# Performance work log

Hardware: AMD Instinct MI355X
Metric: run time of the kernel (lower is better)

## Reference

```python
import jax, jax.numpy as jnp
import numpy as np

WS = 4      # window_size (RSUT5 default)
SHIFT = 2   # window_size // 2
NH = 8      # num_heads
DIM = 256
H0 = W0 = T0 = 32
B0 = 1


def _ln(x, g, b, eps=1e-5):
    m = x.mean(-1, keepdims=True)
    v = ((x - m) ** 2).mean(-1, keepdims=True)
    return (x - m) / jnp.sqrt(v + eps) * g + b


def _rel_index(ws):
    c = np.stack(np.meshgrid(np.arange(ws), np.arange(ws), np.arange(ws), indexing='ij')).reshape(3, -1)
    r = (c[:, :, None] - c[:, None, :]).transpose(1, 2, 0) + (ws - 1)
    return jnp.asarray((r[..., 0] * (2 * ws - 1) + r[..., 1]) * (2 * ws - 1) + r[..., 2])


def _partition(x, ws):
    B, H, W, T, C = x.shape
    x = x.reshape(B, H // ws, ws, W // ws, ws, T // ws, ws, C)
    return x.transpose(0, 1, 3, 5, 2, 4, 6, 7).reshape(-1, ws ** 3, C)


def _reverse(w, ws, B, H, W, T):
    C = w.shape[-1]
    x = w.reshape(B, H // ws, W // ws, T // ws, ws, ws, ws, C)
    return x.transpose(0, 1, 4, 2, 5, 3, 6, 7).reshape(B, H, W, T, C)


def _attn_mask(H, W, T, ws, ss):
    # static (numpy) replica of Block.createmask; H,W,T divisible by ws here
    img = np.zeros((H, W, T), np.float32)
    sls = (slice(0, -ws), slice(-ws, -ss), slice(-ss, None))
    cnt = 0
    for h in sls:
        for w in sls:
            for t in sls:
                img[h, w, t] = cnt
                cnt += 1
    mw = img.reshape(H // ws, ws, W // ws, ws, T // ws, ws).transpose(0, 2, 4, 1, 3, 5).reshape(-1, ws ** 3)
    d = mw[:, None, :] - mw[:, :, None]
    return jnp.asarray(np.where(d != 0, -100.0, 0.0).astype(np.float32))


def _swin(x, H, W, T, shift, mask, n1g, n1b, qkvw, qkvb, rpb, projw, projb, n2g, n2b, fc1w, fc1b, fc2w, fc2b):
    B, L, C = x.shape
    N = WS ** 3
    hd = C // NH
    shortcut = x
    x = _ln(x, n1g, n1b).reshape(B, H, W, T, C)
    if shift:
        x = jnp.roll(x, (-shift, -shift, -shift), axis=(1, 2, 3))
    xw = _partition(x, WS)                                        # [B*nW, N, C]
    qkv = (xw @ qkvw.T + qkvb).reshape(-1, N, 3, NH, hd).transpose(2, 0, 3, 1, 4)
    q, k, v = qkv[0], qkv[1], qkv[2]                              # [B*nW, NH, N, hd]
    attn = jnp.einsum('bhnd,bhmd->bhnm', q * (hd ** -0.5), k)
    attn = attn + rpb[_rel_index(WS)].transpose(2, 0, 1)[None]    # relative position bias
    if mask is not None:
        nW = mask.shape[0]
        attn = (attn.reshape(B, nW, NH, N, N) + mask[None, :, None]).reshape(-1, NH, N, N)
    attn = jax.nn.softmax(attn, axis=-1)
    out = jnp.einsum('bhnm,bhmd->bhnd', attn, v).transpose(0, 2, 1, 3).reshape(-1, N, C)
    out = out @ projw.T + projb
    x = _reverse(out, WS, B, H, W, T)
    if shift:
        x = jnp.roll(x, (shift, shift, shift), axis=(1, 2, 3))
    x = shortcut + x.reshape(B, L, C)
    h = _ln(x, n2g, n2b)
    h = jax.nn.gelu(h @ fc1w.T + fc1b, approximate=False) @ fc2w.T + fc2b
    return x + h


def setup_inputs() -> dict:
    key = jax.random.key(0)
    ks = iter(jax.random.split(key, 16))
    def rn(shape, s=0.02):
        return jax.random.normal(next(ks), shape, jnp.float32) * s
    d = {'x': jax.random.normal(next(ks), (B0, H0 * W0 * T0, DIM), jnp.float32),
         'H': H0, 'W': W0, 'T': T0,
         'norm_g': jnp.ones((DIM,), jnp.float32), 'norm_b': jnp.zeros((DIM,), jnp.float32)}
    for p in ('w', 's'):
        d[p + 'n1g'] = jnp.ones((DIM,), jnp.float32); d[p + 'n1b'] = jnp.zeros((DIM,), jnp.float32)
        d[p + 'qkvw'] = rn((3 * DIM, DIM)); d[p + 'qkvb'] = jnp.zeros((3 * DIM,), jnp.float32)
        d[p + 'rpb'] = rn(((2 * WS - 1) ** 3, NH))
        d[p + 'projw'] = rn((DIM, DIM)); d[p + 'projb'] = jnp.zeros((DIM,), jnp.float32)
        d[p + 'n2g'] = jnp.ones((DIM,), jnp.float32); d[p + 'n2b'] = jnp.zeros((DIM,), jnp.float32)
        d[p + 'fc1w'] = rn((4 * DIM, DIM)); d[p + 'fc1b'] = jnp.zeros((4 * DIM,), jnp.float32)
        d[p + 'fc2w'] = rn((DIM, 4 * DIM)); d[p + 'fc2b'] = jnp.zeros((DIM,), jnp.float32)
    return d


def reference(x, H, W, T, norm_g, norm_b,
              wn1g, wn1b, wqkvw, wqkvb, wrpb, wprojw, wprojb, wn2g, wn2b, wfc1w, wfc1b, wfc2w, wfc2b,
              sn1g, sn1b, sqkvw, sqkvb, srpb, sprojw, sprojb, sn2g, sn2b, sfc1w, sfc1b, sfc2w, sfc2b):
    mask = _attn_mask(H, W, T, WS, SHIFT)
    x = _swin(x, H, W, T, 0, None, wn1g, wn1b, wqkvw, wqkvb, wrpb, wprojw, wprojb, wn2g, wn2b, wfc1w, wfc1b, wfc2w, wfc2b)
    x = _swin(x, H, W, T, SHIFT, mask, sn1g, sn1b, sqkvw, sqkvb, srpb, sprojw, sprojb, sn2g, sn2b, sfc1w, sfc1b, sfc2w, sfc2b)
    B, L, C = x.shape
    # Block.norm + toConv: [B, L, C] -> [B, C, H, W, T]
    return _ln(x, norm_g, norm_b).reshape(B, H, W, T, C).transpose(0, 4, 1, 2, 3)
```

## Files before the change

kernel.cpp:

```cpp
#include <hip/hip_runtime.h>

typedef unsigned short u16;
typedef unsigned int   u32;
typedef __bf16 bfx8 __attribute__((ext_vector_type(8)));
typedef float  fx4  __attribute__((ext_vector_type(4)));

__device__ __forceinline__ u16 f2b(float f) {
    union { float f; u32 i; } v; v.f = f;
    u32 r = (v.i + 0x7fffu + ((v.i >> 16) & 1u)) >> 16;
    return (u16)r;
}
__device__ __forceinline__ u32 pk(float a, float b) {
    return (u32)f2b(a) | ((u32)f2b(b) << 16);
}

__device__ __forceinline__ void gl2lds16(const u16* g, u16* l) {
    __builtin_amdgcn_global_load_lds(
        (const __attribute__((address_space(1))) u32*)(const void*)g,
        (__attribute__((address_space(3))) u32*)(void*)l, 16, 0, 0);
}

__device__ __forceinline__ int map_token(int r, int shift) {
    int win = r >> 6, n = r & 63;
    int wh = win >> 6, ww = (win >> 3) & 7, wt = win & 7;
    int h = wh * 4 + (n >> 4);
    int w = ww * 4 + ((n >> 2) & 3);
    int t = wt * 4 + (n & 3);
    h = (h + shift) & 31; w = (w + shift) & 31; t = (t + shift) & 31;
    return (h << 10) | (w << 5) | t;
}

struct CvtArgs { const float* src[8]; int cum[9]; };
__global__ __launch_bounds__(256) void cvt_kernel(CvtArgs a, u16* __restrict__ dst) {
    int g = (blockIdx.x * 256 + threadIdx.x) * 4;
    int t = 0;
    #pragma unroll
    for (int i = 1; i < 8; i++) t += (g >= a.cum[i]);
    int local = g - a.cum[t];
    float4 f = *(const float4*)(a.src[t] + local);
    uint2 o; o.x = pk(f.x, f.y); o.y = pk(f.z, f.w);
    *(uint2*)(dst + g) = o;
}

template<int GATHER, int F32OUT>
__global__ __launch_bounds__(256) void ln_kernel(const float* __restrict__ resid,
                                                 const float* __restrict__ g, const float* __restrict__ b,
                                                 void* __restrict__ outp, int shift) {
    int lane = threadIdx.x & 63;
    int row  = blockIdx.x * 4 + (threadIdx.x >> 6);
    int src  = GATHER ? map_token(row, shift) : row;
    float4 x = ((const float4*)(resid + src * 256))[lane];
    float s1 = x.x + x.y + x.z + x.w;
    float s2 = x.x * x.x + x.y * x.y + x.z * x.z + x.w * x.w;
    #pragma unroll
    for (int off = 1; off < 64; off <<= 1) { s1 += __shfl_xor(s1, off); s2 += __shfl_xor(s2, off); }
    float mean = s1 * (1.0f / 256.0f);
    float var  = s2 * (1.0f / 256.0f) - mean * mean;
    float rstd = rsqrtf(var + 1e-5f);
    int c = lane * 4;
    float4 gv = *(const float4*)(g + c);
    float4 bv = *(const float4*)(b + c);
    float y0 = (x.x - mean) * rstd * gv.x + bv.x;
    float y1 = (x.y - mean) * rstd * gv.y + bv.y;
    float y2 = (x.z - mean) * rstd * gv.z + bv.z;
    float y3 = (x.w - mean) * rstd * gv.w + bv.w;
    if (F32OUT) {
        float4 o; o.x = y0; o.y = y1; o.z = y2; o.w = y3;
        *(float4*)((float*)outp + row * 256 + c) = o;
    } else {
        uint2 o; o.x = pk(y0, y1); o.y = pk(y2, y3);
        *(uint2*)((u16*)outp + row * 256 + c) = o;
    }
}

template<int EPI>
__global__ __launch_bounds__(256) void gemm2(const u16* __restrict__ A, const u16* __restrict__ W,
                                             const float* __restrict__ bias,
                                             u16* __restrict__ outb, float* __restrict__ resid,
                                             int Nout, int K, int shift) {
    __shared__ u16 As[128 * 32];
    __shared__ u16 Bs[128 * 32];
    int lane = threadIdx.x & 63, w = threadIdx.x >> 6;
    int wm = w >> 1, wn = w & 1;
    int m0 = blockIdx.x * 128, n0 = blockIdx.y * 128;
    int lr = lane & 15, q = lane >> 4;
    int sw = q ^ ((lr >> 1) & 3);

    fx4 acc[4][4] = {};

    for (int kt = 0; kt < K; kt += 32) {
        __syncthreads();
        #pragma unroll
        for (int p = 0; p < 2; p++) {
            int row = p * 64 + w * 16 + (lane >> 2);
            int kg  = (lane & 3) ^ ((row >> 1) & 3);
            int slot = (p * 256 + w * 64 + lane) * 8;
            gl2lds16(A + (size_t)(m0 + row) * K + kt + kg * 8, As + slot);
            gl2lds16(W + (size_t)(n0 + row) * K + kt + kg * 8, Bs + slot);
        }
        __syncthreads();
        bfx8 af[4], bfr[4];
        #pragma unroll
        for (int t = 0; t < 4; t++) {
            int ra = wm * 64 + t * 16 + lr;
            int rb = wn * 64 + t * 16 + lr;
            af[t]  = *(const bfx8*)(As + (ra * 4 + sw) * 8);
            bfr[t] = *(const bfx8*)(Bs + (rb * 4 + sw) * 8);
        }
        #pragma unroll
        for (int i = 0; i < 4; i++)
            #pragma unroll
            for (int j = 0; j < 4; j++)
                acc[i][j] = __builtin_amdgcn_mfma_f32_16x16x32_bf16(af[i], bfr[j], acc[i][j], 0, 0, 0);
    }

    float bv[4];
    #pragma unroll
    for (int j = 0; j < 4; j++) bv[j] = bias[n0 + wn * 64 + j * 16 + lr];
    #pragma unroll
    for (int i = 0; i < 4; i++) {
        #pragma unroll
        for (int r = 0; r < 4; r++) {
            int gr = m0 + wm * 64 + i * 16 + q * 4 + r;
            int orow = (EPI == 3) ? map_token(gr, shift) : gr;
            #pragma unroll
            for (int j = 0; j < 4; j++) {
                int gc = n0 + wn * 64 + j * 16 + lr;
                float v = acc[i][j][r] + bv[j];
                if (EPI == 0) {
                    outb[(size_t)gr * Nout + gc] = f2b(v);
                } else if (EPI == 1) {
                    float gl = 0.5f * v * (1.0f + erff(v * 0.7071067811865476f));
                    outb[(size_t)gr * Nout + gc] = f2b(gl);
                } else {
                    resid[orow * 256 + gc] += v;
                }
            }
        }
    }
}

__global__ __launch_bounds__(128) void attn_mfma(const u16* __restrict__ qkv, const float* __restrict__ rpb,
                                                 u16* __restrict__ outb, int masked) {
    __shared__ u16  Pl[2][64][72];
    __shared__ u16  VT[2][32][72];
    __shared__ float rbS[2][344];
    int w = threadIdx.x >> 6;
    int lane = threadIdx.x & 63;
    int id = blockIdx.x * 2 + w;
    int win = id >> 3, head = id & 7;
    int lr = lane & 15, q = lane >> 4;

    const u16* base = qkv + (size_t)win * 64 * 768 + head * 32;

    bfx8 qf[4], kf[4];
    #pragma unroll
    for (int t = 0; t < 4; t++) {
        const u16* rq = base + (lr + 16 * t) * 768 + q * 8;
        qf[t] = *(const bfx8*)(rq);
        kf[t] = *(const bfx8*)(rq + 256);
    }
    {
        const u16* rv = base + lane * 768 + 512;
        #pragma unroll
        for (int c = 0; c < 32; c += 8) {
            bfx8 vv = *(const bfx8*)(rv + c);
            #pragma unroll
            for (int j = 0; j < 8; j++) VT[w][c + j][lane] = ((const u16*)&vv)[j];
        }
    }
    for (int i = lane; i < 343; i += 64) rbS[w][i] = rpb[i * 8 + head];

    fx4 sT[4][4] = {};
    #pragma unroll
    for (int jt = 0; jt < 4; jt++)
        #pragma unroll
        for (int it = 0; it < 4; it++)
            sT[jt][it] = __builtin_amdgcn_mfma_f32_16x16x32_bf16(kf[jt], qf[it], sT[jt][it], 0, 0, 0);

    int wh = win >> 6, ww = (win >> 3) & 7, wt = win & 7;
    const float scale = 0.17677669529663687f;

    #pragma unroll
    for (int it = 0; it < 4; it++) {
        int i = lr + 16 * it;
        int ih = i >> 4, iw = (i >> 2) & 3, iT = i & 3;
        int labn = 0;
        if (masked) {
            int lh = (wh == 7) ? (1 + (ih >> 1)) : 0;
            int lw = (ww == 7) ? (1 + (iw >> 1)) : 0;
            int lt = (wt == 7) ? (1 + (iT >> 1)) : 0;
            labn = lh * 9 + lw * 3 + lt;
        }
        float sv[4][4];
        float mx = -1e30f;
        #pragma unroll
        for (int jt = 0; jt < 4; jt++)
            #pragma unroll
            for (int r = 0; r < 4; r++) {
                int j = q * 4 + r + 16 * jt;
                int jh = j >> 4, jw = (j >> 2) & 3, jT = j & 3;
                float s = sT[jt][it][r] * scale +
                          rbS[w][((ih - jh + 3) * 7 + (iw - jw + 3)) * 7 + (iT - jT + 3)];
                if (masked) {
                    int lh = (wh == 7) ? (1 + (jh >> 1)) : 0;
                    int lw = (ww == 7) ? (1 + (jw >> 1)) : 0;
                    int lt = (wt == 7) ? (1 + (jT >> 1)) : 0;
                    if (lh * 9 + lw * 3 + lt != labn) s -= 100.0f;
                }
                sv[jt][r] = s;
                mx = fmaxf(mx, s);
            }
        mx = fmaxf(mx, __shfl_xor(mx, 16));
        mx = fmaxf(mx, __shfl_xor(mx, 32));
        float sum = 0.f;
        #pragma unroll
        for (int jt = 0; jt < 4; jt++)
            #pragma unroll
            for (int r = 0; r < 4; r++) { sv[jt][r] = __expf(sv[jt][r] - mx); sum += sv[jt][r]; }
        sum += __shfl_xor(sum, 16);
        sum += __shfl_xor(sum, 32);
        float inv = 1.0f / sum;
        #pragma unroll
        for (int jt = 0; jt < 4; jt++) {
            uint2 pw;
            pw.x = pk(sv[jt][0] * inv, sv[jt][1] * inv);
            pw.y = pk(sv[jt][2] * inv, sv[jt][3] * inv);
            *(uint2*)&Pl[w][i][q * 4 + 16 * jt] = pw;
        }
    }

    fx4 o[4][2] = {};
    #pragma unroll
    for (int kk = 0; kk < 2; kk++) {
        bfx8 pf[4], vf[2];
        #pragma unroll
        for (int it = 0; it < 4; it++) pf[it] = *(const bfx8*)&Pl[w][lr + 16 * it][q * 8 + 32 * kk];
        #pragma unroll
        for (int dt = 0; dt < 2; dt++) vf[dt] = *(const bfx8*)&VT[w][lr + 16 * dt][q * 8 + 32 * kk];
        #pragma unroll
        for (int it = 0; it < 4; it++)
            #pragma unroll
            for (int dt = 0; dt < 2; dt++)
                o[it][dt] = __builtin_amdgcn_mfma_f32_16x16x32_bf16(pf[it], vf[dt], o[it][dt], 0, 0, 0);
    }

    u16* ob = outb + (size_t)win * 64 * 256 + head * 32;
    #pragma unroll
    for (int it = 0; it < 4; it++)
        #pragma unroll
        for (int r = 0; r < 4; r++) {
            int i = 16 * it + q * 4 + r;
            #pragma unroll
            for (int dt = 0; dt < 2; dt++)
                ob[i * 256 + 16 * dt + lr] = f2b(o[it][dt][r]);
        }
}

__global__ __launch_bounds__(256) void transpose_f32(const float* __restrict__ in, float* __restrict__ out) {
    __shared__ float tile[64][65];
    int t0 = blockIdx.x * 64;
    int c0 = blockIdx.y * 64;
    int row = threadIdx.x >> 2, cg = (threadIdx.x & 3) * 16;
    const float* src = in + (t0 + row) * 256 + c0 + cg;
    #pragma unroll
    for (int j = 0; j < 16; j += 4) {
        float4 v = *(const float4*)(src + j);
        tile[row][cg + j] = v.x; tile[row][cg + j + 1] = v.y;
        tile[row][cg + j + 2] = v.z; tile[row][cg + j + 3] = v.w;
    }
    __syncthreads();
    float tmp[16];
    #pragma unroll
    for (int j = 0; j < 16; j++) tmp[j] = tile[cg + j][row];
    float* dst = out + (c0 + row) * 32768 + t0 + cg;
    #pragma unroll
    for (int j = 0; j < 4; j++) *(float4*)(dst + 4 * j) = *(float4*)(tmp + 4 * j);
}

extern "C" void kernel_launch(void* const* d_in, const int* in_sizes, int n_in,
                              void* d_out, int out_size, void* d_ws, size_t ws_size,
                              hipStream_t stream) {
    const float* x      = (const float*)d_in[0];
    const float* norm_g = (const float*)d_in[4];
    const float* norm_b = (const float*)d_in[5];

    char* wsb = (char*)d_ws;
    float* resid = (float*)wsb;
    u16*   xn    = (u16*)(wsb + (size_t)32 * 1024 * 1024);
    u16*   big   = (u16*)(wsb + (size_t)48 * 1024 * 1024);
    u16*   attnb = (u16*)(wsb + (size_t)96 * 1024 * 1024);
    u16*   wb    = (u16*)(wsb + (size_t)112 * 1024 * 1024);
    float* xnf   = (float*)(wsb + (size_t)48 * 1024 * 1024);

    CvtArgs ca;
    static const int offs[9] = {0, 196608, 262144, 524288, 786432, 983040, 1048576, 1310720, 1572864};
    for (int i = 0; i < 9; i++) ca.cum[i] = offs[i];
    ca.src[0] = (const float*)d_in[6 + 2];
    ca.src[1] = (const float*)d_in[6 + 5];
    ca.src[2] = (const float*)d_in[6 + 9];
    ca.src[3] = (const float*)d_in[6 + 11];
    ca.src[4] = (const float*)d_in[19 + 2];
    ca.src[5] = (const float*)d_in[19 + 5];
    ca.src[6] = (const float*)d_in[19 + 9];
    ca.src[7] = (const float*)d_in[19 + 11];
    cvt_kernel<<<1536, 256, 0, stream>>>(ca, wb);

    hipMemcpyAsync(resid, x, (size_t)32768 * 256 * 4, hipMemcpyDeviceToDevice, stream);

    for (int blk = 0; blk < 2; blk++) {
        void* const* P = d_in + 6 + blk * 13;
        const float* n1g  = (const float*)P[0];
        const float* n1b  = (const float*)P[1];
        const float* qkvb = (const float*)P[3];
        const float* rpb  = (const float*)P[4];
        const float* pjb  = (const float*)P[6];
        const float* n2g  = (const float*)P[7];
        const float* n2b  = (const float*)P[8];
        const float* f1b  = (const float*)P[10];
        const float* f2b_ = (const float*)P[12];
        const u16* qkvw = wb + offs[0] + blk * 786432;
        const u16* pjw  = wb + offs[1] + blk * 786432;
        const u16* f1w  = wb + offs[2] + blk * 786432;
        const u16* f2w  = wb + offs[3] + blk * 786432;
        int shift = blk ? 2 : 0;

        ln_kernel<1, 0><<<8192, 256, 0, stream>>>(resid, n1g, n1b, xn, shift);
        gemm2<0><<<dim3(256, 6), 256, 0, stream>>>(xn, qkvw, qkvb, big, nullptr, 768, 256, 0);
        attn_mfma<<<2048, 128, 0, stream>>>(big, rpb, attnb, blk);
        gemm2<3><<<dim3(256, 2), 256, 0, stream>>>(attnb, pjw, pjb, nullptr, resid, 256, 256, shift);
        ln_kernel<0, 0><<<8192, 256, 0, stream>>>(resid, n2g, n2b, xn, 0);
        gemm2<1><<<dim3(256, 8), 256, 0, stream>>>(xn, f1w, f1b, big, nullptr, 1024, 256, 0);
        gemm2<2><<<dim3(256, 2), 256, 0, stream>>>(big, f2w, f2b_, nullptr, resid, 256, 1024, 0);
    }

    ln_kernel<0, 1><<<8192, 256, 0, stream>>>(resid, norm_g, norm_b, xnf, 0);
    transpose_f32<<<dim3(512, 4), 256, 0, stream>>>(xnf, (float*)d_out);
}
```

Baseline: 520.0 us.

## Fuse final layernorm with transpose, drop residual memcpy, use tanh-form GELU

Merges the final LayerNorm and the channel-first transpose into one kernel that normalizes 32 tokens per block and writes transposed through a skewed LDS tile. This removes the intermediate fp32 buffer round trip. The initial device-to-device copy of x into the residual buffer is also removed: the first block reads x directly and the projection epilogue writes resid = src + v. The erf GELU is replaced by a tanh-style approximation using exp and a fast reciprocal, which changes numerics slightly.

```diff
diff --git a/kernel.cpp b/kernel.cpp
--- a/kernel.cpp
+++ b/kernel.cpp
@@ -28,6 +28,13 @@
     int t = wt * 4 + (n & 3);
     h = (h + shift) & 31; w = (w + shift) & 31; t = (t + shift) & 31;
     return (h << 10) | (w << 5) | t;
+}
+
+__device__ __forceinline__ float gelu_fast(float v) {
+    float t = v * v;
+    float u = v * __builtin_fmaf(t, 0.044715f, 1.0f);
+    float e = __expf(-1.5957691216057308f * u);
+    return v * __builtin_amdgcn_rcpf(1.0f + e);
 }
 
 struct CvtArgs { const float* src[8]; int cum[9]; };
@@ -77,7 +84,8 @@
 __global__ __launch_bounds__(256) void gemm2(const u16* __restrict__ A, const u16* __restrict__ W,
                                              const float* __restrict__ bias,
                                              u16* __restrict__ outb, float* __restrict__ resid,
-                                             int Nout, int K, int shift) {
+                                             int Nout, int K, int shift,
+                                             const float* __restrict__ rsrc) {
     __shared__ u16 As[128 * 32];
     __shared__ u16 Bs[128 * 32];
     int lane = threadIdx.x & 63, w = threadIdx.x >> 6;
@@ -130,10 +138,9 @@
                 if (EPI == 0) {
                     outb[(size_t)gr * Nout + gc] = f2b(v);
                 } else if (EPI == 1) {
-                    float gl = 0.5f * v * (1.0f + erff(v * 0.7071067811865476f));
-                    outb[(size_t)gr * Nout + gc] = f2b(gl);
+                    outb[(size_t)gr * Nout + gc] = f2b(gelu_fast(v));
                 } else {
-                    resid[orow * 256 + gc] += v;
+                    resid[orow * 256 + gc] = rsrc[orow * 256 + gc] + v;
                 }
             }
         }
@@ -257,25 +264,56 @@
         }
 }
 
-__global__ __launch_bounds__(256) void transpose_f32(const float* __restrict__ in, float* __restrict__ out) {
-    __shared__ float tile[64][65];
-    int t0 = blockIdx.x * 64;
-    int c0 = blockIdx.y * 64;
-    int row = threadIdx.x >> 2, cg = (threadIdx.x & 3) * 16;
-    const float* src = in + (t0 + row) * 256 + c0 + cg;
-    #pragma unroll
-    for (int j = 0; j < 16; j += 4) {
-        float4 v = *(const float4*)(src + j);
-        tile[row][cg + j] = v.x; tile[row][cg + j + 1] = v.y;
-        tile[row][cg + j + 2] = v.z; tile[row][cg + j + 3] = v.w;
+__global__ __launch_bounds__(256) void ln_tr(const float* __restrict__ in,
+                                             const float* __restrict__ g, const float* __restrict__ b,
+                                             float* __restrict__ out) {
+    __shared__ float tile[256 * 33];
+    int tid = threadIdx.x;
+    int r   = tid >> 3;
+    int cg  = (tid & 7) * 32;
+    int row = blockIdx.x * 32 + r;
+    const float* src = in + (size_t)row * 256 + cg;
+
+    float v[32];
+    float s1 = 0.f, s2 = 0.f;
+    #pragma unroll
+    for (int j = 0; j < 8; j++) {
+        float4 f = *(const float4*)(src + 4 * j);
+        v[4*j] = f.x; v[4*j+1] = f.y; v[4*j+2] = f.z; v[4*j+3] = f.w;
+        s1 += f.x + f.y + f.z + f.w;
+        s2 += f.x*f.x + f.y*f.y + f.z*f.z + f.w*f.w;
+    }
+    #pragma unroll
+    for (int off = 1; off < 8; off <<= 1) { s1 += __shfl_xor(s1, off); s2 += __shfl_xor(s2, off); }
+    float mean = s1 * (1.0f / 256.0f);
+    float rstd = rsqrtf(s2 * (1.0f / 256.0f) - mean * mean + 1e-5f);
+
+    #pragma unroll
+    for (int j = 0; j < 8; j++) {
+        float4 gv = *(const float4*)(g + cg + 4 * j);
+        float4 bv = *(const float4*)(b + cg + 4 * j);
+        int c0 = cg + 4 * j;
+        int slot = (r + (c0 >> 2)) & 31;
+        tile[(c0 + 0) * 33 + slot] = (v[4*j]   - mean) * rstd * gv.x + bv.x;
+        tile[(c0 + 1) * 33 + slot] = (v[4*j+1] - mean) * rstd * gv.y + bv.y;
+        tile[(c0 + 2) * 33 + slot] = (v[4*j+2] - mean) * rstd * gv.z + bv.z;
+        tile[(c0 + 3) * 33 + slot] = (v[4*j+3] - mean) * rstd * gv.w + bv.w;
     }
     __syncthreads();
-    float tmp[16];
-    #pragma unroll
-    for (int j = 0; j < 16; j++) tmp[j] = tile[cg + j][row];
-    float* dst = out + (c0 + row) * 32768 + t0 + cg;
-    #pragma unroll
-    for (int j = 0; j < 4; j++) *(float4*)(dst + 4 * j) = *(float4*)(tmp + 4 * j);
+
+    int c = tid;
+    int csh = (c >> 2) & 31;
+    const float* base = &tile[c * 33];
+    float o[32];
+    #pragma unroll
+    for (int r2 = 0; r2 < 32; r2++) o[r2] = base[(r2 + csh) & 31];
+
+    float* dst = out + (size_t)c * 32768 + blockIdx.x * 32;
+    #pragma unroll
+    for (int j = 0; j < 8; j++) {
+        float4 f; f.x = o[4*j]; f.y = o[4*j+1]; f.z = o[4*j+2]; f.w = o[4*j+3];
+        *(float4*)(dst + 4 * j) = f;
+    }
 }
 
 extern "C" void kernel_launch(void* const* d_in, const int* in_sizes, int n_in,
@@ -291,7 +329,6 @@
     u16*   big   = (u16*)(wsb + (size_t)48 * 1024 * 1024);
     u16*   attnb = (u16*)(wsb + (size_t)96 * 1024 * 1024);
     u16*   wb    = (u16*)(wsb + (size_t)112 * 1024 * 1024);
-    float* xnf   = (float*)(wsb + (size_t)48 * 1024 * 1024);
 
     CvtArgs ca;
     static const int offs[9] = {0, 196608, 262144, 524288, 786432, 983040, 1048576, 1310720, 1572864};
@@ -305,8 +342,6 @@
     ca.src[6] = (const float*)d_in[19 + 9];
     ca.src[7] = (const float*)d_in[19 + 11];
     cvt_kernel<<<1536, 256, 0, stream>>>(ca, wb);
-
-    hipMemcpyAsync(resid, x, (size_t)32768 * 256 * 4, hipMemcpyDeviceToDevice, stream);
 
     for (int blk = 0; blk < 2; blk++) {
         void* const* P = d_in + 6 + blk * 13;
@@ -325,15 +360,17 @@
         const u16* f2w  = wb + offs[3] + blk * 786432;
         int shift = blk ? 2 : 0;
 
-        ln_kernel<1, 0><<<8192, 256, 0, stream>>>(resid, n1g, n1b, xn, shift);
-        gemm2<0><<<dim3(256, 6), 256, 0, stream>>>(xn, qkvw, qkvb, big, nullptr, 768, 256, 0);
+        const float* ln1src = blk ? resid : x;
+        const float* projadd = blk ? resid : x;
+
+        ln_kernel<1, 0><<<8192, 256, 0, stream>>>(ln1src, n1g, n1b, xn, shift);
+        gemm2<0><<<dim3(256, 6), 256, 0, stream>>>(xn, qkvw, qkvb, big, nullptr, 768, 256, 0, nullptr);
         attn_mfma<<<2048, 128, 0, stream>>>(big, rpb, attnb, blk);
-        gemm2<3><<<dim3(256, 2), 256, 0, stream>>>(attnb, pjw, pjb, nullptr, resid, 256, 256, shift);
+        gemm2<3><<<dim3(256, 2), 256, 0, stream>>>(attnb, pjw, pjb, nullptr, resid, 256, 256, shift, projadd);
         ln_kernel<0, 0><<<8192, 256, 0, stream>>>(resid, n2g, n2b, xn, 0);
-        gemm2<1><<<dim3(256, 8), 256, 0, stream>>>(xn, f1w, f1b, big, nullptr, 1024, 256, 0);
-        gemm2<2><<<dim3(256, 2), 256, 0, stream>>>(big, f2w, f2b_, nullptr, resid, 256, 1024, 0);
-    }
-
-    ln_kernel<0, 1><<<8192, 256, 0, stream>>>(resid, norm_g, norm_b, xnf, 0);
-    transpose_f32<<<dim3(512, 4), 256, 0, stream>>>(xnf, (float*)d_out);
-}
+        gemm2<1><<<dim3(256, 8), 256, 0, stream>>>(xn, f1w, f1b, big, nullptr, 1024, 256, 0, nullptr);
+        gemm2<2><<<dim3(256, 2), 256, 0, stream>>>(big, f2w, f2b_, nullptr, resid, 256, 1024, 0, resid);
+    }
+
+    ln_tr<<<1024, 256, 0, stream>>>(resid, norm_g, norm_b, (float*)d_out);
+}
```

After: 480.5 us. 1.08x faster.
